# Performance work log

Measured on AMD Instinct MI355X. Metric: run time of the kernel, lower is better.

## Reference

```python
import jax, jax.numpy as jnp
import numpy as np

N_NODES = 50000
N_EDGES = 640000
IN_CH = 128
HIDDEN = 128
HEADS = 4
HEAD_DIM = HIDDEN // HEADS  # 32
NEG_SLOPE = 0.2


def setup_inputs() -> dict:
    key = jax.random.key(0)
    ks = jax.random.split(key, 12)
    x = jax.random.normal(ks[0], (N_NODES, IN_CH), dtype=jnp.float32)
    edge_index = jax.random.randint(ks[1], (2, N_EDGES), 0, N_NODES, dtype=jnp.int64)
    s = 0.1
    W1 = jax.random.normal(ks[2], (IN_CH, HEADS * HEAD_DIM), dtype=jnp.float32) * s
    a_src1 = jax.random.normal(ks[3], (HEADS, HEAD_DIM), dtype=jnp.float32) * s
    a_dst1 = jax.random.normal(ks[4], (HEADS, HEAD_DIM), dtype=jnp.float32) * s
    b1 = jax.random.normal(ks[5], (HEADS * HEAD_DIM,), dtype=jnp.float32) * s
    W2 = jax.random.normal(ks[6], (HIDDEN, HEADS * HEAD_DIM), dtype=jnp.float32) * s
    a_src2 = jax.random.normal(ks[7], (HEADS, HEAD_DIM), dtype=jnp.float32) * s
    a_dst2 = jax.random.normal(ks[8], (HEADS, HEAD_DIM), dtype=jnp.float32) * s
    b2 = jax.random.normal(ks[9], (HEADS * HEAD_DIM,), dtype=jnp.float32) * s
    return {"x": x, "edge_index": edge_index, "W1": W1, "a_src1": a_src1,
            "a_dst1": a_dst1, "b1": b1, "W2": W2, "a_src2": a_src2,
            "a_dst2": a_dst2, "b2": b2}


def _gat_conv(x, src, dst, W, a_src, a_dst, b):
    """PyG GATConv (concat=True, add_self_loops already applied to src/dst)."""
    N = x.shape[0]
    H, C = a_src.shape
    h = (x @ W).reshape(N, H, C)                      # [N, H, C]
    alpha_s = jnp.einsum('nhc,hc->nh', h, a_src)      # [N, H]
    alpha_d = jnp.einsum('nhc,hc->nh', h, a_dst)      # [N, H]
    e = alpha_s[src] + alpha_d[dst]                   # [E, H]
    e = jnp.where(e > 0, e, NEG_SLOPE * e)            # leaky_relu(0.2)
    # segment softmax over destination nodes (every node has a self-loop)
    emax = jax.ops.segment_max(e, dst, num_segments=N)
    ee = jnp.exp(e - emax[dst])
    denom = jax.ops.segment_sum(ee, dst, num_segments=N)
    alpha = ee / (denom[dst] + 1e-16)                 # [E, H]
    out = jax.ops.segment_sum(h[src] * alpha[:, :, None], dst, num_segments=N)
    return out.reshape(N, H * C) + b


def reference(x, edge_index, W1, a_src1, a_dst1, b1, W2, a_src2, a_dst2, b2):
    N = x.shape[0]
    loops = jnp.arange(N, dtype=edge_index.dtype)
    src = jnp.concatenate([edge_index[0], loops])
    dst = jnp.concatenate([edge_index[1], loops])
    h = _gat_conv(x, src, dst, W1, a_src1, a_dst1, b1)
    h = jax.nn.relu(h)  # dropout is identity in eval mode
    out = _gat_conv(h, src, dst, W2, a_src2, a_dst2, b2)
    return out
```

## Files before the change

kernel.cpp:

```cpp
#include <hip/hip_runtime.h>
#include <hip/hip_bf16.h>
#include <hip/hip_fp16.h>

#define N_NODES 50000
#define N_EDGES 640000
#define E_TOT   690000
#define CH      128
#define ROWPAD  50176
#define GEMMB   391
#define EBLK    2048
#define NEB     337
#define NBUCK   196
#define CAP     4608

typedef __attribute__((ext_vector_type(8))) short short8;
typedef __attribute__((ext_vector_type(4))) float float4v;

static __device__ __forceinline__ float bf2f(unsigned short u) {
  return __uint_as_float(((unsigned)u) << 16);
}
static __device__ __forceinline__ unsigned short f2bf(float f) {
  unsigned u = __float_as_uint(f);
  return (unsigned short)((u + 0x7fffu + ((u >> 16) & 1u)) >> 16);
}

static __device__ __forceinline__ void load_edge(const int* __restrict__ ei,
                                                 int e, int i64, int& s, int& d)
{
  if (e >= N_EDGES) { s = d = e - N_EDGES; return; }
  if (i64) { s = ei[2 * (size_t)e]; d = ei[2 * ((size_t)N_EDGES + e)]; }
  else     { s = ei[e];             d = ei[N_EDGES + e]; }
}

static __device__ __forceinline__ short8 load_bf8(const void* __restrict__ X,
                                                  size_t off, int f32)
{
  if (!f32) return *(const short8*)((const unsigned short*)X + off);
  const float4* p = (const float4*)((const float*)X + off);
  float4 u = p[0], v = p[1];
  short8 r;
  r[0] = (short)f2bf(u.x); r[1] = (short)f2bf(u.y);
  r[2] = (short)f2bf(u.z); r[3] = (short)f2bf(u.w);
  r[4] = (short)f2bf(v.x); r[5] = (short)f2bf(v.y);
  r[6] = (short)f2bf(v.z); r[7] = (short)f2bf(v.w);
  return r;
}

__global__ __launch_bounds__(256) void k_prep(
    const void* __restrict__ W1, const void* __restrict__ W2,
    const void* __restrict__ as1, const void* __restrict__ ad1,
    const void* __restrict__ as2, const void* __restrict__ ad2,
    unsigned short* __restrict__ Wt1, unsigned short* __restrict__ Wt2,
    unsigned short* __restrict__ Ba1, unsigned short* __restrict__ Ba2,
    const unsigned short* __restrict__ x16,
    const unsigned int* __restrict__ eiw,
    int* __restrict__ flags, int* __restrict__ gcur)
{
  int b = blockIdx.x, t = threadIdx.x;
  __shared__ int sf, si;
  if (t == 0) { sf = 0; si = 1; }
  __syncthreads();
  int bad = 0;
  for (int i = t; i < 4096; i += 256) {
    float v = bf2f(x16[i]);
    if (!(v == v) || fabsf(v) > 100.f) bad = 1;
  }
  if (bad) atomicOr(&sf, 1);
  if (b == 0 && t < 128 && eiw[2 * t + 1] != 0u) atomicAnd(&si, 0);
  __syncthreads();
  int f32 = sf;
  if (b == 0 && t == 0) { flags[0] = sf; flags[1] = si; }
  if (b == 0 && t < NBUCK) gcur[t] = t * CAP;

  if (b < 8) {
    int g = b * 256 + t;
    int l = g >> 10;
    int rem = g & 1023;
    int k = rem >> 3, n = rem & 7;
    const void* W  = l ? W2 : W1;
    const void* av = (n < 4) ? (l ? as2 : as1) : (l ? ad2 : ad1);
    int h = n & 3;
    float sum = 0.f;
    for (int c = 0; c < 32; c++) {
      float w = f32 ? ((const float*)W)[k * 128 + h * 32 + c]
                    : bf2f(((const unsigned short*)W)[k * 128 + h * 32 + c]);
      float a = f32 ? ((const float*)av)[h * 32 + c]
                    : bf2f(((const unsigned short*)av)[h * 32 + c]);
      sum += w * a;
    }
    unsigned short* Ba = l ? Ba2 : Ba1;
    Ba[n * 128 + k] = f2bf(sum);
    Ba[(8 + (rem >> 7)) * 128 + (rem & 127)] = 0;
  } else {
    int b2 = b - 8;
    int l = b2 >> 7, c = b2 & 127;
    if (t < 128) {
      const void* W = l ? W2 : W1;
      unsigned short* Wt = l ? Wt2 : Wt1;
      Wt[c * 128 + t] = f32 ? f2bf(((const float*)W)[t * 128 + c])
                            : ((const unsigned short*)W)[t * 128 + c];
    }
  }
}

struct SmemG { unsigned short WB[144][136]; };

static __device__ __forceinline__ void gemm_body(
    SmemG& sm, int bx,
    const void* __restrict__ X,
    const unsigned short* __restrict__ Wt_g,
    const unsigned short* __restrict__ Ba_g,
    unsigned short* __restrict__ H, float* __restrict__ AS,
    float* __restrict__ AD, int nrows, int xf32)
{
  int tid = threadIdx.x;
#pragma unroll
  for (int i = 0; i < 8; i++) {
    int j = i * 256 + tid;
    int c = j >> 4, k8 = j & 15;
    *(short8*)&sm.WB[c][k8 * 8] = *(const short8*)(Wt_g + c * 128 + k8 * 8);
  }
  {
    int n = tid >> 4, k8 = tid & 15;
    *(short8*)&sm.WB[128 + n][k8 * 8] = *(const short8*)(Ba_g + n * 128 + k8 * 8);
  }
  __syncthreads();
  int wave = tid >> 6, lane = tid & 63;
  int R0 = (bx * 4 + wave) * 32;
  if (R0 >= nrows) return;
  int m = lane & 15, quad = lane >> 4;
  int rA = R0 + m;        if (rA >= nrows) rA = nrows - 1;
  int rB = R0 + 16 + m;   if (rB >= nrows) rB = nrows - 1;
  size_t aA = (size_t)rA * CH + quad * 8;
  size_t aB = (size_t)rB * CH + quad * 8;
  float4v acc[2][8];
  float4v accA[2];
#pragma unroll
  for (int hf = 0; hf < 2; hf++) {
    accA[hf] = (float4v){0.f, 0.f, 0.f, 0.f};
#pragma unroll
    for (int ct = 0; ct < 8; ct++) acc[hf][ct] = (float4v){0.f, 0.f, 0.f, 0.f};
  }
#pragma unroll
  for (int kb = 0; kb < 4; kb++) {
    short8 a0 = load_bf8(X, aA + kb * 32, xf32);
    short8 a1 = load_bf8(X, aB + kb * 32, xf32);
#pragma unroll
    for (int ct = 0; ct < 8; ct++) {
      short8 bb = *(const short8*)&sm.WB[ct * 16 + m][kb * 32 + quad * 8];
      acc[0][ct] = __builtin_amdgcn_mfma_f32_16x16x32_bf16(a0, bb, acc[0][ct], 0, 0, 0);
      acc[1][ct] = __builtin_amdgcn_mfma_f32_16x16x32_bf16(a1, bb, acc[1][ct], 0, 0, 0);
    }
    short8 bA = *(const short8*)&sm.WB[128 + m][kb * 32 + quad * 8];
    accA[0] = __builtin_amdgcn_mfma_f32_16x16x32_bf16(a0, bA, accA[0], 0, 0, 0);
    accA[1] = __builtin_amdgcn_mfma_f32_16x16x32_bf16(a1, bA, accA[1], 0, 0, 0);
  }
#pragma unroll
  for (int hf = 0; hf < 2; hf++) {
    int rbase = R0 + hf * 16 + quad * 4;
#pragma unroll
    for (int ct = 0; ct < 8; ct++) {
      int col = ct * 16 + m;
#pragma unroll
      for (int r = 0; r < 4; r++)
        H[(size_t)(rbase + r) * CH + col] = __half_as_ushort(__float2half(acc[hf][ct][r]));
    }
    if (m < 4) {
#pragma unroll
      for (int r = 0; r < 4; r++)
        AS[(size_t)(rbase + r) * 4 + m] = accA[hf][r];
    } else if (m < 8) {
#pragma unroll
      for (int r = 0; r < 4; r++)
        AD[(size_t)(rbase + r) * 4 + (m - 4)] = accA[hf][r];
    }
  }
}

__global__ __launch_bounds__(256, 2) void k_gemm(
    const void* __restrict__ X,
    const unsigned short* __restrict__ Wt_g,
    const unsigned short* __restrict__ Ba_g,
    unsigned short* __restrict__ H, float* __restrict__ AS, float* __restrict__ AD,
    int nrows)
{
  __shared__ SmemG sm;
  gemm_body(sm, blockIdx.x, X, Wt_g, Ba_g, H, AS, AD, nrows, 0);
}

__global__ __launch_bounds__(256, 2) void k_gemm_scat(
    const void* __restrict__ X,
    const unsigned short* __restrict__ Wt_g,
    const unsigned short* __restrict__ Ba_g,
    unsigned short* __restrict__ H, float* __restrict__ AS, float* __restrict__ AD,
    int nrows, const int* __restrict__ ei, int* __restrict__ gcur,
    unsigned int* __restrict__ ebuf, const int* __restrict__ flags)
{
  __shared__ SmemG sm;
  __shared__ int hist[NBUCK];
  __shared__ int cur[NBUCK];
  if (blockIdx.x >= GEMMB) {
    int b = blockIdx.x - GEMMB;
    int t = threadIdx.x;
    if (t < NBUCK) hist[t] = 0;
    __syncthreads();
    int i64 = flags[1];
    int base = b * EBLK;
    int sA[8], dA[8];
#pragma unroll
    for (int k = 0; k < 8; k++) {
      int e = base + k * 256 + t;
      sA[k] = -1;
      if (e < E_TOT) {
        load_edge(ei, e, i64, sA[k], dA[k]);
        atomicAdd(&hist[dA[k] >> 8], 1);
      }
    }
    __syncthreads();
    if (t < NBUCK) {
      int c = hist[t];
      cur[t] = c ? atomicAdd(&gcur[t], c) : 0;
    }
    __syncthreads();
#pragma unroll
    for (int k = 0; k < 8; k++) {
      if (sA[k] >= 0) {
        int pos = atomicAdd(&cur[dA[k] >> 8], 1);
        ebuf[pos] = ((unsigned)sA[k] << 8) | (unsigned)(dA[k] & 255);
      }
    }
    return;
  }
  gemm_body(sm, blockIdx.x, X, Wt_g, Ba_g, H, AS, AD, nrows, flags[0]);
}

__global__ __launch_bounds__(256) void k_fine(
    const unsigned int* __restrict__ ebuf, const int* __restrict__ gcur,
    int2* __restrict__ rpdeg, unsigned short* __restrict__ csr)
{
  __shared__ int cnt[256], sh[256], cur[256];
  int q = blockIdx.x, t = threadIdx.x;
  int lo = q * CAP, hi = gcur[q];
  cnt[t] = 0;
  __syncthreads();
  for (int i = lo + t; i < hi; i += 256)
    atomicAdd(&cnt[ebuf[i] & 255u], 1);
  __syncthreads();
  int v = cnt[t];
  sh[t] = v;
  __syncthreads();
  for (int off = 1; off < 256; off <<= 1) {
    int u = (t >= off) ? sh[t - off] : 0;
    __syncthreads();
    sh[t] += u;
    __syncthreads();
  }
  int lp = sh[t] - v;
  int n = (q << 8) + t;
  if (n < N_NODES) rpdeg[n] = make_int2(lo + lp, v);
  cur[t] = lo + lp;
  __syncthreads();
  for (int i = lo + t; i < hi; i += 256) {
    unsigned p = ebuf[i];
    int slot = atomicAdd(&cur[p & 255u], 1);
    csr[slot] = (unsigned short)(p >> 8);
  }
}

__global__ __launch_bounds__(256, 8) void k_agg(
    const int2* __restrict__ rpdeg,
    const unsigned short* __restrict__ csr,
    const __half* __restrict__ H,
    const float* __restrict__ AS, const float* __restrict__ AD,
    const void* __restrict__ b, void* __restrict__ Y,
    const int* __restrict__ flags, int layer)
{
  int tid = threadIdx.x;
  int node = blockIdx.x * 4 + (tid >> 6);
  if (node >= N_NODES) return;
  int lane = tid & 63;
  int h = lane >> 4;
  int c0 = 2 * lane;
  int2 rd = rpdeg[node];
  int start = rd.x, dg = rd.y;
  float adh = AD[node * 4 + h];
  const __half2* __restrict__ H2 = (const __half2*)H;
  float accx = 0.f, accy = 0.f, den = 0.f;
  for (int j = 0; j < dg; j += 8) {
    int sI[8];
#pragma unroll
    for (int u = 0; u < 8; u++) {
      int idx = j + u;
      idx = idx < dg ? idx : dg - 1;
      sI[u] = (int)csr[start + idx];
    }
    __half2 vV[8];
#pragma unroll
    for (int u = 0; u < 8; u++)
      vV[u] = H2[sI[u] * 64 + lane];
    float eV[8];
#pragma unroll
    for (int u = 0; u < 8; u++)
      eV[u] = AS[sI[u] * 4 + h] + adh;
#pragma unroll
    for (int u = 0; u < 8; u++) {
      float x = eV[u] > 0.f ? eV[u] : 0.2f * eV[u];
      float ex = (j + u < dg) ? __expf(x) : 0.f;
      float2 v = __half22float2(vV[u]);
      accx += ex * v.x;
      accy += ex * v.y;
      den  += ex;
    }
  }
  float inv = 1.f / (den + 1e-16f);
  int f32 = flags[0];
  float b0 = f32 ? ((const float*)b)[c0]     : bf2f(((const unsigned short*)b)[c0]);
  float b1 = f32 ? ((const float*)b)[c0 + 1] : bf2f(((const unsigned short*)b)[c0 + 1]);
  float r0 = accx * inv + b0;
  float r1 = accy * inv + b1;
  int o = node * CH + c0;
  if (layer == 1) {
    r0 = r0 > 0.f ? r0 : 0.f;
    r1 = r1 > 0.f ? r1 : 0.f;
    ushort2 w; w.x = f2bf(r0); w.y = f2bf(r1);
    *(ushort2*)((unsigned short*)Y + o) = w;
  } else if (f32) {
    float2 w; w.x = r0; w.y = r1;
    *(float2*)((float*)Y + o) = w;
  } else {
    ushort2 w; w.x = f2bf(r0); w.y = f2bf(r1);
    *(ushort2*)((unsigned short*)Y + o) = w;
  }
}

extern "C" void kernel_launch(void* const* d_in, const int* in_sizes, int n_in,
                              void* d_out, int out_size, void* d_ws, size_t ws_size,
                              hipStream_t stream)
{
  const void* x   = d_in[0];
  const int*  ei  = (const int*)d_in[1];
  const void* W1  = d_in[2];
  const void* as1 = d_in[3];
  const void* ad1 = d_in[4];
  const void* b1  = d_in[5];
  const void* W2  = d_in[6];
  const void* as2 = d_in[7];
  const void* ad2 = d_in[8];
  const void* b2  = d_in[9];

  char* ws = (char*)d_ws;
  unsigned short* H   = (unsigned short*)(ws);
  float*  AS          = (float*)(ws + 12845056);
  float*  AD          = (float*)(ws + 13647872);
  unsigned short* X2  = (unsigned short*)(ws + 14450688);
  int2*   rpdeg       = (int2*)(ws + 27295744);
  unsigned short* csr = (unsigned short*)(ws + 27695744);
  unsigned int* ebuf  = (unsigned int*)(ws + 29502080);
  int*    gcur        = (int*)(ws + 33114752);
  int*    flags       = (int*)(ws + 33115648);
  unsigned short* Wt1 = (unsigned short*)(ws + 33116672);
  unsigned short* Wt2 = (unsigned short*)(ws + 33149440);
  unsigned short* Ba1 = (unsigned short*)(ws + 33182208);
  unsigned short* Ba2 = (unsigned short*)(ws + 33186304);

  const int agg_blocks = (N_NODES + 3) / 4;

  k_prep<<<264, 256, 0, stream>>>(W1, W2, as1, ad1, as2, ad2,
                                  Wt1, Wt2, Ba1, Ba2,
                                  (const unsigned short*)x,
                                  (const unsigned int*)ei, flags, gcur);

  k_gemm_scat<<<GEMMB + NEB, 256, 0, stream>>>(
      x, Wt1, Ba1, H, AS, AD, N_NODES, ei, gcur, ebuf, flags);

  k_fine<<<NBUCK, 256, 0, stream>>>(ebuf, gcur, rpdeg, csr);

  k_agg<<<agg_blocks, 256, 0, stream>>>(rpdeg, csr,
                                        (const __half*)H, AS, AD,
                                        b1, X2, flags, 1);

  k_gemm<<<GEMMB, 256, 0, stream>>>(X2, Wt2, Ba2, H, AS, AD, N_NODES);
  k_agg<<<agg_blocks, 256, 0, stream>>>(rpdeg, csr,
                                        (const __half*)H, AS, AD,
                                        b2, d_out, flags, 2);
}
```

Measured before the change: 202.8 us.

## Pad CSR segments to 8 and aggregate with 32 lanes per node

The CSR builder now pads each node's neighbour list to a multiple of 8 in a larger per-bucket region and zero-fills that region, so the aggregation kernel can read 8 indices with one 16-byte vector load and needs no clamping. The aggregation kernel maps one node to 32 lanes with 4 channels each, using 8-byte feature gathers and wider stores, and processes 8 nodes per block. Padding entries point at node 0 and are masked out by the degree check. This adds zero-fill work and CSR footprint, and moves the workspace offsets to fit.

```diff
diff --git a/kernel.cpp b/kernel.cpp
--- a/kernel.cpp
+++ b/kernel.cpp
@@ -12,6 +12,7 @@
 #define NEB     337
 #define NBUCK   196
 #define CAP     4608
+#define CAPC    6144
 
 typedef __attribute__((ext_vector_type(8))) short short8;
 typedef __attribute__((ext_vector_type(4))) float float4v;
@@ -241,13 +242,16 @@
   __shared__ int cnt[256], sh[256], cur[256];
   int q = blockIdx.x, t = threadIdx.x;
   int lo = q * CAP, hi = gcur[q];
+  int lc = q * CAPC;
   cnt[t] = 0;
+  for (int i = lc + t; i < lc + CAPC; i += 256) csr[i] = 0;
   __syncthreads();
   for (int i = lo + t; i < hi; i += 256)
     atomicAdd(&cnt[ebuf[i] & 255u], 1);
   __syncthreads();
   int v = cnt[t];
-  sh[t] = v;
+  int a = (v + 7) & ~7;
+  sh[t] = a;
   __syncthreads();
   for (int off = 1; off < 256; off <<= 1) {
     int u = (t >= off) ? sh[t - off] : 0;
@@ -255,10 +259,10 @@
     sh[t] += u;
     __syncthreads();
   }
-  int lp = sh[t] - v;
+  int lpa = sh[t] - a;
   int n = (q << 8) + t;
-  if (n < N_NODES) rpdeg[n] = make_int2(lo + lp, v);
-  cur[t] = lo + lp;
+  if (n < N_NODES) rpdeg[n] = make_int2(lc + lpa, v);
+  cur[t] = lc + lpa;
   __syncthreads();
   for (int i = lo + t; i < hi; i += 256) {
     unsigned p = ebuf[i];
@@ -270,66 +274,79 @@
 __global__ __launch_bounds__(256, 8) void k_agg(
     const int2* __restrict__ rpdeg,
     const unsigned short* __restrict__ csr,
-    const __half* __restrict__ H,
+    const unsigned short* __restrict__ H,
     const float* __restrict__ AS, const float* __restrict__ AD,
     const void* __restrict__ b, void* __restrict__ Y,
     const int* __restrict__ flags, int layer)
 {
   int tid = threadIdx.x;
-  int node = blockIdx.x * 4 + (tid >> 6);
+  int node = blockIdx.x * 8 + (tid >> 5);
   if (node >= N_NODES) return;
-  int lane = tid & 63;
-  int h = lane >> 4;
-  int c0 = 2 * lane;
+  int lane = tid & 31;
+  int h = lane >> 3;
+  int c0 = 4 * lane;
   int2 rd = rpdeg[node];
   int start = rd.x, dg = rd.y;
   float adh = AD[node * 4 + h];
-  const __half2* __restrict__ H2 = (const __half2*)H;
-  float accx = 0.f, accy = 0.f, den = 0.f;
+  float acc0 = 0.f, acc1 = 0.f, acc2 = 0.f, acc3 = 0.f, den = 0.f;
   for (int j = 0; j < dg; j += 8) {
+    short8 sv = *(const short8*)(csr + start + j);
     int sI[8];
 #pragma unroll
+    for (int u = 0; u < 8; u++) sI[u] = ((int)sv[u]) & 0xFFFF;
+    float2 vR[8];
+#pragma unroll
+    for (int u = 0; u < 8; u++)
+      vR[u] = *(const float2*)(H + (sI[u] << 7) + c0);
+    float eV[8];
+#pragma unroll
+    for (int u = 0; u < 8; u++)
+      eV[u] = AS[(sI[u] << 2) + h] + adh;
+#pragma unroll
     for (int u = 0; u < 8; u++) {
-      int idx = j + u;
-      idx = idx < dg ? idx : dg - 1;
-      sI[u] = (int)csr[start + idx];
-    }
-    __half2 vV[8];
-#pragma unroll
-    for (int u = 0; u < 8; u++)
-      vV[u] = H2[sI[u] * 64 + lane];
-    float eV[8];
-#pragma unroll
-    for (int u = 0; u < 8; u++)
-      eV[u] = AS[sI[u] * 4 + h] + adh;
-#pragma unroll
-    for (int u = 0; u < 8; u++) {
-      float x = eV[u] > 0.f ? eV[u] : 0.2f * eV[u];
+      float x = eV[u];
+      x = fmaxf(x, 0.2f * x);
       float ex = (j + u < dg) ? __expf(x) : 0.f;
-      float2 v = __half22float2(vV[u]);
-      accx += ex * v.x;
-      accy += ex * v.y;
+      __half2 p0 = __builtin_bit_cast(__half2, vR[u].x);
+      __half2 p1 = __builtin_bit_cast(__half2, vR[u].y);
+      float2 f0 = __half22float2(p0);
+      float2 f1 = __half22float2(p1);
+      acc0 += ex * f0.x;
+      acc1 += ex * f0.y;
+      acc2 += ex * f1.x;
+      acc3 += ex * f1.y;
       den  += ex;
     }
   }
   float inv = 1.f / (den + 1e-16f);
   int f32 = flags[0];
-  float b0 = f32 ? ((const float*)b)[c0]     : bf2f(((const unsigned short*)b)[c0]);
-  float b1 = f32 ? ((const float*)b)[c0 + 1] : bf2f(((const unsigned short*)b)[c0 + 1]);
-  float r0 = accx * inv + b0;
-  float r1 = accy * inv + b1;
+  float b0, b1, b2, b3;
+  if (f32) {
+    const float* bp = (const float*)b;
+    b0 = bp[c0]; b1 = bp[c0 + 1]; b2 = bp[c0 + 2]; b3 = bp[c0 + 3];
+  } else {
+    const unsigned short* bp = (const unsigned short*)b;
+    b0 = bf2f(bp[c0]); b1 = bf2f(bp[c0 + 1]);
+    b2 = bf2f(bp[c0 + 2]); b3 = bf2f(bp[c0 + 3]);
+  }
+  float r0 = acc0 * inv + b0;
+  float r1 = acc1 * inv + b1;
+  float r2 = acc2 * inv + b2;
+  float r3 = acc3 * inv + b3;
   int o = node * CH + c0;
   if (layer == 1) {
-    r0 = r0 > 0.f ? r0 : 0.f;
-    r1 = r1 > 0.f ? r1 : 0.f;
-    ushort2 w; w.x = f2bf(r0); w.y = f2bf(r1);
-    *(ushort2*)((unsigned short*)Y + o) = w;
+    r0 = r0 > 0.f ? r0 : 0.f;  r1 = r1 > 0.f ? r1 : 0.f;
+    r2 = r2 > 0.f ? r2 : 0.f;  r3 = r3 > 0.f ? r3 : 0.f;
+    ushort4 w;
+    w.x = f2bf(r0); w.y = f2bf(r1); w.z = f2bf(r2); w.w = f2bf(r3);
+    *(ushort4*)((unsigned short*)Y + o) = w;
   } else if (f32) {
-    float2 w; w.x = r0; w.y = r1;
-    *(float2*)((float*)Y + o) = w;
+    float4 w; w.x = r0; w.y = r1; w.z = r2; w.w = r3;
+    *(float4*)((float*)Y + o) = w;
   } else {
-    ushort2 w; w.x = f2bf(r0); w.y = f2bf(r1);
-    *(ushort2*)((unsigned short*)Y + o) = w;
+    ushort4 w;
+    w.x = f2bf(r0); w.y = f2bf(r1); w.z = f2bf(r2); w.w = f2bf(r3);
+    *(ushort4*)((unsigned short*)Y + o) = w;
   }
 }
 
@@ -355,15 +372,15 @@
   unsigned short* X2  = (unsigned short*)(ws + 14450688);
   int2*   rpdeg       = (int2*)(ws + 27295744);
   unsigned short* csr = (unsigned short*)(ws + 27695744);
-  unsigned int* ebuf  = (unsigned int*)(ws + 29502080);
-  int*    gcur        = (int*)(ws + 33114752);
-  int*    flags       = (int*)(ws + 33115648);
-  unsigned short* Wt1 = (unsigned short*)(ws + 33116672);
-  unsigned short* Wt2 = (unsigned short*)(ws + 33149440);
-  unsigned short* Ba1 = (unsigned short*)(ws + 33182208);
-  unsigned short* Ba2 = (unsigned short*)(ws + 33186304);
-
-  const int agg_blocks = (N_NODES + 3) / 4;
+  unsigned int* ebuf  = (unsigned int*)(ws + 30104192);
+  int*    gcur        = (int*)(ws + 33716864);
+  int*    flags       = (int*)(ws + 33718016);
+  unsigned short* Wt1 = (unsigned short*)(ws + 33719040);
+  unsigned short* Wt2 = (unsigned short*)(ws + 33751808);
+  unsigned short* Ba1 = (unsigned short*)(ws + 33784576);
+  unsigned short* Ba2 = (unsigned short*)(ws + 33788672);
+
+  const int agg_blocks = (N_NODES + 7) / 8;
 
   k_prep<<<264, 256, 0, stream>>>(W1, W2, as1, ad1, as2, ad2,
                                   Wt1, Wt2, Ba1, Ba2,
@@ -375,12 +392,10 @@
 
   k_fine<<<NBUCK, 256, 0, stream>>>(ebuf, gcur, rpdeg, csr);
 
-  k_agg<<<agg_blocks, 256, 0, stream>>>(rpdeg, csr,
-                                        (const __half*)H, AS, AD,
+  k_agg<<<agg_blocks, 256, 0, stream>>>(rpdeg, csr, H, AS, AD,
                                         b1, X2, flags, 1);
 
   k_gemm<<<GEMMB, 256, 0, stream>>>(X2, Wt2, Ba2, H, AS, AD, N_NODES);
-  k_agg<<<agg_blocks, 256, 0, stream>>>(rpdeg, csr,
-                                        (const __half*)H, AS, AD,
+  k_agg<<<agg_blocks, 256, 0, stream>>>(rpdeg, csr, H, AS, AD,
                                         b2, d_out, flags, 2);
 }
```

After: 195.0 us. 3.9% less time.
